# Kernel tuning notes

Hardware: AMD Instinct MI355X
Metric: run time of the kernel (lower is better)

The kernel has to match this reference:

```python
import jax, jax.numpy as jnp
import numpy as np

DIM = 1024
H = 16
DH = DIM // H
SCALE = DH ** -0.5
EPS = 1e-5


def _linear_params(key, fan_in, fan_out):
    k1, k2 = jax.random.split(key)
    bound = 1.0 / np.sqrt(fan_in)
    w = jax.random.uniform(k1, (fan_out, fan_in), jnp.float32, -bound, bound)
    b = jax.random.uniform(k2, (fan_out,), jnp.float32, -bound, bound)
    return w, b


def setup_inputs() -> dict:
    key = jax.random.key(0)
    ks = jax.random.split(key, 16)
    M, K, S_txt, S_img = 32, 128, 1024, 768
    inp = {
        'entity_text': jax.random.normal(ks[0], (M, K, DIM), jnp.float32),
        'entity_image': jax.random.normal(ks[1], (M, K, DIM), jnp.float32),
        'img_feat': jax.random.normal(ks[2], (M, S_img, DIM), jnp.float32),
        'txt_feat': jax.random.normal(ks[3], (M, S_txt, DIM), jnp.float32),
    }
    img_mask = jax.random.randint(ks[4], (M, S_img), 0, 2, jnp.int32)
    txt_mask = jax.random.randint(ks[5], (M, S_txt), 0, 2, jnp.int32)
    # guarantee at least one valid kv token per row (avoids all -inf rows)
    inp['img_mask'] = img_mask.at[:, 0].set(1)
    inp['txt_mask'] = txt_mask.at[:, 0].set(1)
    names = ['wq_t', 'wk_t', 'wv_t', 'wo_t', 'wq_i', 'wk_i', 'wv_i', 'wo_i']
    for i, n in enumerate(names):
        w, b = _linear_params(ks[6 + i], DIM, DIM)
        inp[n] = w
        inp['b' + n[1:]] = b
    inp['g_t'] = jnp.ones((DIM,), jnp.float32)
    inp['beta_t'] = jnp.zeros((DIM,), jnp.float32)
    inp['g_i'] = jnp.ones((DIM,), jnp.float32)
    inp['beta_i'] = jnp.zeros((DIM,), jnp.float32)
    return inp


def _attend(wq, bq, wk, bk, wv, bv, wo, bo, queries, kv, kv_mask):
    M, K, D = queries.shape
    S = kv.shape[1]
    Q = (queries @ wq.T + bq).reshape(M, K, H, DH)
    Kt = (kv @ wk.T + bk).reshape(M, S, H, DH)
    V = (kv @ wv.T + bv).reshape(M, S, H, DH)
    attn = jnp.einsum('mkhd,mshd->mhks', Q, Kt) * SCALE  # [M,H,K,S]
    attn = jnp.where(kv_mask[:, None, None, :] > 0, attn, -jnp.inf)
    attn = jax.nn.softmax(attn, axis=-1)
    attn = jnp.nan_to_num(attn, nan=0.0)  # dropout=eval mode (identity)
    out = jnp.einsum('mhks,mshd->mkhd', attn, V).reshape(M, K, D)
    return out @ wo.T + bo


def _layernorm(x, g, b):
    mu = jnp.mean(x, axis=-1, keepdims=True)
    var = jnp.mean(jnp.square(x - mu), axis=-1, keepdims=True)
    return (x - mu) * jax.lax.rsqrt(var + EPS) * g + b


def reference(entity_text, entity_image, img_feat, txt_feat, img_mask, txt_mask,
              wq_t, bq_t, wk_t, bk_t, wv_t, bv_t, wo_t, bo_t,
              wq_i, bq_i, wk_i, bk_i, wv_i, bv_i, wo_i, bo_i,
              g_t, beta_t, g_i, beta_i):
    out_t = _attend(wq_t, bq_t, wk_t, bk_t, wv_t, bv_t, wo_t, bo_t,
                    entity_text, txt_feat, txt_mask)
    out_i = _attend(wq_i, bq_i, wk_i, bk_i, wv_i, bv_i, wo_i, bo_i,
                    entity_image, img_feat, img_mask)
    et = _layernorm(entity_text + out_t, g_t, beta_t)
    ei = _layernorm(entity_image + out_i, g_i, beta_i)
    return (et, ei)
```

## Files before the change

### kernel.cpp

```cpp
#include <hip/hip_runtime.h>
#include <stdint.h>

typedef unsigned short u16;
typedef __attribute__((ext_vector_type(8))) short short8;
typedef __attribute__((ext_vector_type(4))) float f32x4;

#define SWZ(r) (((r) & 7) << 4)
#define SWZV(dr) ((((dr) & 7) ^ (((dr) >> 3) & 7)) << 4)
#define SCALE 0.125f

__device__ __forceinline__ u16 f2bf(float f) {
  unsigned int x = __float_as_uint(f);
  x += 0x7fffu + ((x >> 16) & 1u);
  return (u16)(x >> 16);
}

__device__ __forceinline__ unsigned int cvtpk_bf16(float lo, float hi) {
  unsigned int r;
  asm("v_cvt_pk_bf16_f32 %0, %1, %2" : "=v"(r) : "v"(lo), "v"(hi));
  return r;
}

__device__ __forceinline__ f32x4 mfma16(short8 a, short8 b, f32x4 c) {
  return __builtin_amdgcn_mfma_f32_16x16x32_bf16(a, b, c, 0, 0, 0);
}

__device__ __forceinline__ void gload_lds16(const u16* g, u16* l) {
  __builtin_amdgcn_global_load_lds(
      (const __attribute__((address_space(1))) unsigned int*)g,
      (__attribute__((address_space(3))) unsigned int*)l, 16, 0, 0);
}

__device__ __forceinline__ int xcd_swz(int bid, int nwg) {
  int cpx = nwg >> 3;
  return (bid & 7) * cpx + (bid >> 3);
}

__device__ __forceinline__ void cvt8(const float* src, u16* dst) {
  f32x4 a = __builtin_nontemporal_load((const f32x4*)src);
  f32x4 b = __builtin_nontemporal_load((const f32x4*)(src + 4));
  uint4 u;
  u.x = cvtpk_bf16(a[0], a[1]);
  u.y = cvtpk_bf16(a[2], a[3]);
  u.z = cvtpk_bf16(b[0], b[1]);
  u.w = cvtpk_bf16(b[2], b[3]);
  *(uint4*)dst = u;
}

__global__ __launch_bounds__(256) void cvt_all_kernel(
    const float* __restrict__ w0, const float* __restrict__ w1,
    const float* __restrict__ w2, const float* __restrict__ w3,
    const float* __restrict__ ent, const float* __restrict__ feat,
    u16* __restrict__ Wbf, u16* __restrict__ entbf, u16* __restrict__ featbf,
    int nE8, int nF8) {
  const int nW8 = 524288;
  int total = nW8 + nE8 + nF8;
  int i = blockIdx.x * 256 + threadIdx.x;
  int stride = gridDim.x * 256;
  for (; i < total; i += stride) {
    if (i < nW8) {
      int mi = i >> 17;
      const float* s = (mi == 0) ? w0 : (mi == 1) ? w1 : (mi == 2) ? w2 : w3;
      size_t off = (size_t)(i & 131071) * 8;
      cvt8(s + off, Wbf + (size_t)mi * 1048576 + off);
    } else if (i < nW8 + nE8) {
      size_t off = (size_t)(i - nW8) * 8;
      cvt8(ent + off, entbf + off);
    } else {
      size_t off = (size_t)(i - nW8 - nE8) * 8;
      cvt8(feat + off, featbf + off);
    }
  }
}

__global__ __launch_bounds__(256) void cvt_a_kernel(
    const float* __restrict__ src, u16* __restrict__ dst, int n8) {
  int i = blockIdx.x * 256 + threadIdx.x;
  int stride = gridDim.x * 256;
  for (; i < n8; i += stride) cvt8(src + (size_t)i * 8, dst + (size_t)i * 8);
}

__device__ __forceinline__ void gemm_core_bf16(
    const u16* __restrict__ A, const u16* __restrict__ B,
    const float* __restrict__ bias0, const float* __restrict__ bias1,
    u16* __restrict__ C, int ldc, int bx, int by, u16* As, u16* Bs) {
  const int tid = threadIdx.x;
  const int lane = tid & 63;
  const int w = tid >> 6;
  const int wr = w >> 1, wc = w & 1;
  const int l15 = lane & 15, lg = lane >> 4;
  const int brow = by * 128;
  const int bcol = bx * 128;

  f32x4 acc[4][4] = {};

  for (int k0 = 0; k0 < 1024; k0 += 64) {
#pragma unroll
    for (int p = 0; p < 4; ++p) {
      int flat = p * 256 + tid;
      int row = flat >> 3;
      int cb = (flat & 7) * 16;
      int scb = cb ^ SWZ(row);
      gload_lds16(B + (size_t)(bcol + row) * 1024 + k0 + (scb >> 1),
                  Bs + (size_t)flat * 8);
    }
#pragma unroll
    for (int p = 0; p < 4; ++p) {
      int flat = p * 256 + tid;
      int row = flat >> 3;
      int cb = (flat & 7) * 16;
      int scb = cb ^ SWZ(row);
      gload_lds16(A + (size_t)(brow + row) * 1024 + k0 + (scb >> 1),
                  As + (size_t)flat * 8);
    }
    __syncthreads();

    short8 af[4][2], bfr[4][2];
#pragma unroll
    for (int i = 0; i < 4; ++i) {
#pragma unroll
      for (int kk = 0; kk < 2; ++kk) {
        int ar = wr * 64 + i * 16 + l15;
        af[i][kk] = *(const short8*)((const char*)As + ar * 128 +
                                     ((kk * 64 + lg * 16) ^ SWZ(ar)));
        int br = wc * 64 + i * 16 + l15;
        bfr[i][kk] = *(const short8*)((const char*)Bs + br * 128 +
                                      ((kk * 64 + lg * 16) ^ SWZ(br)));
      }
    }
#pragma unroll
    for (int i = 0; i < 4; ++i)
#pragma unroll
      for (int j = 0; j < 4; ++j)
#pragma unroll
        for (int kk = 0; kk < 2; ++kk)
          acc[i][j] = mfma16(af[i][kk], bfr[j][kk], acc[i][j]);
    __syncthreads();
  }

#pragma unroll
  for (int j = 0; j < 4; ++j) {
    int col = bcol + wc * 64 + j * 16 + l15;
    const float* bp = (col < 1024) ? bias0 : bias1;
    float bv = bp[col & 1023];
#pragma unroll
    for (int i = 0; i < 4; ++i) {
      int row0 = brow + wr * 64 + i * 16 + lg * 4;
#pragma unroll
      for (int r = 0; r < 4; ++r)
        C[(size_t)(row0 + r) * ldc + col] = f2bf(acc[i][j][r] + bv);
    }
  }
}

__global__ __launch_bounds__(256, 2) void qkv_gemm_kernel(
    const u16* __restrict__ A0, const u16* __restrict__ B0,
    const float* __restrict__ bq, u16* __restrict__ C0, int gx0, int nwg0,
    const u16* __restrict__ A1, const u16* __restrict__ B1,
    const float* __restrict__ bk, const float* __restrict__ bv,
    u16* __restrict__ C1, int gx1, int nwg1) {
  __shared__ __attribute__((aligned(16))) u16 As[128 * 64];
  __shared__ __attribute__((aligned(16))) u16 Bs[128 * 64];
  int bid = blockIdx.x;
  if (bid < nwg0) {
    int lid = xcd_swz(bid, nwg0);
    gemm_core_bf16(A0, B0, bq, bq, C0, 1024, lid % gx0, lid / gx0, As, Bs);
  } else {
    int lid = xcd_swz(bid - nwg0, nwg1);
    gemm_core_bf16(A1, B1, bk, bv, C1, 2048, lid % gx1, lid / gx1, As, Bs);
  }
}

template <bool A_F32, bool OUT_F32>
__global__ __launch_bounds__(256, 2) void gemm_bias_kernel(
    const void* __restrict__ Av, const u16* __restrict__ B,
    const float* __restrict__ bias0, const float* __restrict__ bias1,
    void* __restrict__ Cv, int ldc) {
  __shared__ __attribute__((aligned(16))) u16 As[128 * 64];
  __shared__ __attribute__((aligned(16))) u16 Bs[128 * 64];
  const int tid = threadIdx.x;
  const int lane = tid & 63;
  const int w = tid >> 6;
  const int wr = w >> 1, wc = w & 1;
  const int l15 = lane & 15, lg = lane >> 4;

  const int nwg = gridDim.x * gridDim.y;
  const int lid = xcd_swz(blockIdx.y * gridDim.x + blockIdx.x, nwg);
  const int bx = lid % gridDim.x;
  const int by = lid / gridDim.x;
  const int brow = by * 128;
  const int bcol = bx * 128;

  f32x4 acc[4][4] = {};

  for (int k0 = 0; k0 < 1024; k0 += 64) {
#pragma unroll
    for (int p = 0; p < 4; ++p) {
      int flat = p * 256 + tid;
      int row = flat >> 3;
      int cb = (flat & 7) * 16;
      int scb = cb ^ SWZ(row);
      gload_lds16(B + (size_t)(bcol + row) * 1024 + k0 + (scb >> 1),
                  Bs + (size_t)flat * 8);
    }
    if constexpr (A_F32) {
      const float* Af = (const float*)Av;
#pragma unroll
      for (int p = 0; p < 4; ++p) {
        int flat = p * 256 + tid;
        int row = flat >> 3;
        int c8 = flat & 7;
        const float* src = Af + (size_t)(brow + row) * 1024 + k0 + c8 * 8;
        float4 v0 = ((const float4*)src)[0];
        float4 v1 = ((const float4*)src)[1];
        uint4 u;
        u.x = cvtpk_bf16(v0.x, v0.y);
        u.y = cvtpk_bf16(v0.z, v0.w);
        u.z = cvtpk_bf16(v1.x, v1.y);
        u.w = cvtpk_bf16(v1.z, v1.w);
        *(uint4*)((char*)As + row * 128 + ((c8 * 16) ^ SWZ(row))) = u;
      }
    } else {
      const u16* Ab = (const u16*)Av;
#pragma unroll
      for (int p = 0; p < 4; ++p) {
        int flat = p * 256 + tid;
        int row = flat >> 3;
        int cb = (flat & 7) * 16;
        int scb = cb ^ SWZ(row);
        gload_lds16(Ab + (size_t)(brow + row) * 1024 + k0 + (scb >> 1),
                    As + (size_t)flat * 8);
      }
    }
    __syncthreads();

    short8 af[4][2], bfr[4][2];
#pragma unroll
    for (int i = 0; i < 4; ++i) {
#pragma unroll
      for (int kk = 0; kk < 2; ++kk) {
        int ar = wr * 64 + i * 16 + l15;
        af[i][kk] = *(const short8*)((const char*)As + ar * 128 +
                                     ((kk * 64 + lg * 16) ^ SWZ(ar)));
        int br = wc * 64 + i * 16 + l15;
        bfr[i][kk] = *(const short8*)((const char*)Bs + br * 128 +
                                      ((kk * 64 + lg * 16) ^ SWZ(br)));
      }
    }
#pragma unroll
    for (int i = 0; i < 4; ++i)
#pragma unroll
      for (int j = 0; j < 4; ++j)
#pragma unroll
        for (int kk = 0; kk < 2; ++kk)
          acc[i][j] = mfma16(af[i][kk], bfr[j][kk], acc[i][j]);
    __syncthreads();
  }

#pragma unroll
  for (int j = 0; j < 4; ++j) {
    int col = bcol + wc * 64 + j * 16 + l15;
    const float* bp = (col < 1024) ? bias0 : bias1;
    float bv = bp[col & 1023];
#pragma unroll
    for (int i = 0; i < 4; ++i) {
      int row0 = brow + wr * 64 + i * 16 + lg * 4;
#pragma unroll
      for (int r = 0; r < 4; ++r) {
        float v = acc[i][j][r] + bv;
        if constexpr (OUT_F32)
          ((float*)Cv)[(size_t)(row0 + r) * ldc + col] = v;
        else
          ((u16*)Cv)[(size_t)(row0 + r) * ldc + col] = f2bf(v);
      }
    }
  }
}

__global__ __launch_bounds__(256, 2) void attn_mfma_kernel(
    const u16* __restrict__ Q, const u16* __restrict__ KV,
    const int* __restrict__ mask, u16* __restrict__ AO, int S, int mbase) {
  __shared__ __attribute__((aligned(16))) u16 Ks[64 * 64];
  __shared__ __attribute__((aligned(16))) u16 Vt[64 * 64];
  __shared__ __attribute__((aligned(16))) u16 Ps[4 * 32 * 64];
  __shared__ float mb[64];

  const int tid = threadIdx.x;
  const int lane = tid & 63;
  const int w = tid >> 6;
  const int lid = xcd_swz(blockIdx.x, gridDim.x);
  const int ml = lid >> 4;
  const int h = lid & 15;
  const int mg = mbase + ml;
  const int l15 = lane & 15, lg = lane >> 4;

  short8 qf[2][2];
#pragma unroll
  for (int qb = 0; qb < 2; ++qb)
#pragma unroll
    for (int kk = 0; kk < 2; ++kk)
      qf[qb][kk] = *(const short8*)(Q + (size_t)(mg * 128 + w * 32 + qb * 16 + l15) * 1024 +
                                    h * 64 + kk * 32 + lg * 8);

  float mrun[2][4], lrun[2][4];
  f32x4 oacc[2][4] = {};
#pragma unroll
  for (int qb = 0; qb < 2; ++qb)
#pragma unroll
    for (int r = 0; r < 4; ++r) {
      mrun[qb][r] = -1e30f;
      lrun[qb][r] = 0.0f;
    }

  const size_t kvbase = (size_t)ml * S * 2048 + h * 64;

  for (int st = 0; st < S; st += 64) {
    if (tid < 64)
      mb[tid] = (mask[(size_t)mg * S + st + tid] > 0) ? 0.0f : -1e30f;
#pragma unroll
    for (int p = 0; p < 2; ++p) {
      int flat = p * 256 + tid;
      int row = flat >> 3;
      int c = flat & 7;
      short8 v = *(const short8*)(KV + kvbase + (size_t)(st + row) * 2048 + c * 8);
      *(short8*)((char*)Ks + row * 128 + ((c * 16) ^ SWZ(row))) = v;
    }
    {
      int sp = (tid >> 3) * 2;
      int c = tid & 7;
      const u16* src = KV + kvbase + 1024 + (size_t)(st + sp) * 2048 + c * 8;
      short8 v0 = *(const short8*)(src);
      short8 v1 = *(const short8*)(src + 2048);
#pragma unroll
      for (int j = 0; j < 8; ++j) {
        int dr = c * 8 + j;
        unsigned int val = (unsigned int)(u16)v0[j] | ((unsigned int)(u16)v1[j] << 16);
        *(unsigned int*)((char*)Vt + dr * 128 + ((sp * 2) ^ SWZV(dr))) = val;
      }
    }
    __syncthreads();

    short8 kf[4][2];
#pragma unroll
    for (int sb = 0; sb < 4; ++sb)
#pragma unroll
      for (int kk = 0; kk < 2; ++kk) {
        int row = sb * 16 + l15;
        kf[sb][kk] = *(const short8*)((const char*)Ks + row * 128 +
                                      ((kk * 64 + lg * 16) ^ SWZ(row)));
      }
    f32x4 sc[2][4] = {};
#pragma unroll
    for (int qb = 0; qb < 2; ++qb)
#pragma unroll
      for (int sb = 0; sb < 4; ++sb)
#pragma unroll
        for (int kk = 0; kk < 2; ++kk)
          sc[qb][sb] = mfma16(qf[qb][kk], kf[sb][kk], sc[qb][sb]);

    float mbv[4];
#pragma unroll
    for (int sb = 0; sb < 4; ++sb) mbv[sb] = mb[sb * 16 + l15];

#pragma unroll
    for (int qb = 0; qb < 2; ++qb) {
#pragma unroll
      for (int r = 0; r < 4; ++r) {
        float s0 = sc[qb][0][r] * SCALE + mbv[0];
        float s1 = sc[qb][1][r] * SCALE + mbv[1];
        float s2 = sc[qb][2][r] * SCALE + mbv[2];
        float s3 = sc[qb][3][r] * SCALE + mbv[3];
        float t = fmaxf(fmaxf(s0, s1), fmaxf(s2, s3));
        for (int d = 1; d < 16; d <<= 1) t = fmaxf(t, __shfl_xor(t, d));
        float mnew = fmaxf(mrun[qb][r], t);
        float resc = __expf(mrun[qb][r] - mnew);
        float p0 = __expf(s0 - mnew);
        float p1 = __expf(s1 - mnew);
        float p2 = __expf(s2 - mnew);
        float p3 = __expf(s3 - mnew);
        float rs = p0 + p1 + p2 + p3;
        for (int d = 1; d < 16; d <<= 1) rs += __shfl_xor(rs, d);
        lrun[qb][r] = lrun[qb][r] * resc + rs;
        mrun[qb][r] = mnew;
#pragma unroll
        for (int db = 0; db < 4; ++db) oacc[qb][db][r] *= resc;
        int row = qb * 16 + lg * 4 + r;
        char* pbase = (char*)Ps + (w * 32 + row) * 128;
        int colb = 2 * l15;
        *(u16*)(pbase + ((0 * 32 + colb) ^ SWZ(row))) = f2bf(p0);
        *(u16*)(pbase + ((1 * 32 + colb) ^ SWZ(row))) = f2bf(p1);
        *(u16*)(pbase + ((2 * 32 + colb) ^ SWZ(row))) = f2bf(p2);
        *(u16*)(pbase + ((3 * 32 + colb) ^ SWZ(row))) = f2bf(p3);
      }
    }
    asm volatile("" ::: "memory");

    short8 pf[2][2], vf[4][2];
#pragma unroll
    for (int qb = 0; qb < 2; ++qb)
#pragma unroll
      for (int kk = 0; kk < 2; ++kk) {
        int row = qb * 16 + l15;
        pf[qb][kk] = *(const short8*)((const char*)Ps + (w * 32 + row) * 128 +
                                      ((kk * 64 + lg * 16) ^ SWZ(row)));
      }
#pragma unroll
    for (int db = 0; db < 4; ++db)
#pragma unroll
      for (int kk = 0; kk < 2; ++kk) {
        int row = db * 16 + l15;
        vf[db][kk] = *(const short8*)((const char*)Vt + row * 128 +
                                      ((kk * 64 + lg * 16) ^ SWZV(row)));
      }
#pragma unroll
    for (int qb = 0; qb < 2; ++qb)
#pragma unroll
      for (int db = 0; db < 4; ++db)
#pragma unroll
        for (int kk = 0; kk < 2; ++kk)
          oacc[qb][db] = mfma16(pf[qb][kk], vf[db][kk], oacc[qb][db]);
    __syncthreads();
  }

#pragma unroll
  for (int qb = 0; qb < 2; ++qb)
#pragma unroll
    for (int db = 0; db < 4; ++db)
#pragma unroll
      for (int r = 0; r < 4; ++r) {
        int grow = mg * 128 + w * 32 + qb * 16 + lg * 4 + r;
        int gcol = h * 64 + db * 16 + l15;
        float v = oacc[qb][db][r] / lrun[qb][r];
        AO[(size_t)grow * 1024 + gcol] = f2bf(v);
      }
}

__global__ __launch_bounds__(256) void ln_kernel(
    const float* __restrict__ X, const float* __restrict__ O,
    const float* __restrict__ g, const float* __restrict__ b,
    float* __restrict__ out) {
  int row = blockIdx.x;
  int tid = threadIdx.x;
  const float* xr = X + (size_t)row * 1024;
  const float* orr = O + (size_t)row * 1024;
  float4 xv = *(const float4*)(xr + tid * 4);
  float4 ov = *(const float4*)(orr + tid * 4);
  float v0 = xv.x + ov.x, v1 = xv.y + ov.y, v2 = xv.z + ov.z, v3 = xv.w + ov.w;
  float s = v0 + v1 + v2 + v3;
  float s2 = v0 * v0 + v1 * v1 + v2 * v2 + v3 * v3;
  for (int d = 1; d < 64; d <<= 1) {
    s += __shfl_xor(s, d);
    s2 += __shfl_xor(s2, d);
  }
  __shared__ float ps[4], ps2[4];
  int w = tid >> 6;
  if ((tid & 63) == 0) {
    ps[w] = s;
    ps2[w] = s2;
  }
  __syncthreads();
  s = ps[0] + ps[1] + ps[2] + ps[3];
  s2 = ps2[0] + ps2[1] + ps2[2] + ps2[3];
  float mu = s * (1.0f / 1024.0f);
  float var = s2 * (1.0f / 1024.0f) - mu * mu;
  float rstd = rsqrtf(var + 1e-5f);
  float4 gv = *(const float4*)(g + tid * 4);
  float4 bv = *(const float4*)(b + tid * 4);
  float4 ou;
  ou.x = (v0 - mu) * rstd * gv.x + bv.x;
  ou.y = (v1 - mu) * rstd * gv.y + bv.y;
  ou.z = (v2 - mu) * rstd * gv.z + bv.z;
  ou.w = (v3 - mu) * rstd * gv.w + bv.w;
  *(float4*)(out + (size_t)row * 1024 + tid * 4) = ou;
}

extern "C" void kernel_launch(void* const* d_in, const int* in_sizes, int n_in,
                              void* d_out, int out_size, void* d_ws, size_t ws_size,
                              hipStream_t stream) {
  const float* ent_t = (const float*)d_in[0];
  const float* ent_i = (const float*)d_in[1];
  const float* img_feat = (const float*)d_in[2];
  const float* txt_feat = (const float*)d_in[3];
  const int* img_mask = (const int*)d_in[4];
  const int* txt_mask = (const int*)d_in[5];
  const float* W[8];
  const float* Bv[8];
  for (int i = 0; i < 8; ++i) {
    W[i] = (const float*)d_in[6 + 2 * i];
    Bv[i] = (const float*)d_in[7 + 2 * i];
  }
  const float* g_t = (const float*)d_in[22];
  const float* beta_t = (const float*)d_in[23];
  const float* g_i = (const float*)d_in[24];
  const float* beta_i = (const float*)d_in[25];
  float* out = (float*)d_out;

  int nc = 0;
  size_t Xt = 0;
  for (int t = 1; t <= 4; t <<= 1) {
    size_t x = 134217728ull / t;
    if ((32ull << 20) + x + x / 2 <= ws_size) { nc = t; Xt = x; break; }
  }

  char* ws = (char*)d_ws;
  u16* Wbf = (u16*)ws;
  u16* Qbf = (u16*)(ws + (8ull << 20));
  u16* AObf = (u16*)(ws + (16ull << 20));

  if (nc > 0) {
    u16* entbf = (u16*)(ws + (24ull << 20));
    u16* KVc = (u16*)(ws + (32ull << 20));
    u16* featbf = (u16*)(ws + (32ull << 20) + Xt);
    float* Of32 = (float*)(ws + (32ull << 20));
    const int mpc = 32 / nc;

    for (int mod = 0; mod < 2; ++mod) {
      const float* ent = mod ? ent_i : ent_t;
      const float* feat = mod ? img_feat : txt_feat;
      const int* msk = mod ? img_mask : txt_mask;
      int S = mod ? 768 : 1024;
      int crows = mpc * S;

      const u16* wq = Wbf;
      const u16* wkv = Wbf + 1ull * 1048576;
      const u16* wo = Wbf + 3ull * 1048576;

      cvt_all_kernel<<<2048, 256, 0, stream>>>(
          W[mod * 4 + 0], W[mod * 4 + 1], W[mod * 4 + 2], W[mod * 4 + 3],
          ent, feat, Wbf, entbf, featbf, 4096 * 128, crows * 128);

      for (int c = 0; c < nc; ++c) {
        if (c > 0) {
          const float* featc = feat + (size_t)c * mpc * S * 1024;
          cvt_a_kernel<<<2048, 256, 0, stream>>>(featc, featbf, crows * 128);
        }
        int nwg0 = (c == 0) ? 256 : 0;
        int nwg1 = 16 * (crows / 128);
        qkv_gemm_kernel<<<nwg0 + nwg1, 256, 0, stream>>>(
            entbf, wq, Bv[mod * 4 + 0], Qbf, 8, nwg0,
            featbf, wkv, Bv[mod * 4 + 1], Bv[mod * 4 + 2], KVc, 16, nwg1);
        attn_mfma_kernel<<<mpc * 16, 256, 0, stream>>>(Qbf, KVc, msk, AObf, S, c * mpc);
      }

      gemm_bias_kernel<false, true><<<dim3(8, 32), 256, 0, stream>>>(
          AObf, wo, Bv[mod * 4 + 3], Bv[mod * 4 + 3], Of32, 1024);
      ln_kernel<<<4096, 256, 0, stream>>>(ent, Of32,
                                          mod ? g_i : g_t, mod ? beta_i : beta_t,
                                          out + (size_t)mod * 4194304);
    }
  } else {
    int ncf = 4;
    if (ws_size >= (152ull << 20)) ncf = 1;
    else if (ws_size >= (88ull << 20)) ncf = 2;
    u16* KVc = (u16*)(ws + (24ull << 20));
    float* Of32 = (float*)(ws + (24ull << 20));
    const int mpc = 32 / ncf;

    for (int mod = 0; mod < 2; ++mod) {
      const float* ent = mod ? ent_i : ent_t;
      const float* feat = mod ? img_feat : txt_feat;
      const int* msk = mod ? img_mask : txt_mask;
      int S = mod ? 768 : 1024;

      cvt_all_kernel<<<2048, 256, 0, stream>>>(
          W[mod * 4 + 0], W[mod * 4 + 1], W[mod * 4 + 2], W[mod * 4 + 3],
          ent, ent, Wbf, Qbf, Qbf, 0, 0);

      const u16* wq = Wbf;
      const u16* wkv = Wbf + 1ull * 1048576;
      const u16* wo = Wbf + 3ull * 1048576;

      gemm_bias_kernel<true, false><<<dim3(8, 32), 256, 0, stream>>>(
          ent, wq, Bv[mod * 4 + 0], Bv[mod * 4 + 0], Qbf, 1024);

      int crows = mpc * S;
      for (int c = 0; c < ncf; ++c) {
        const float* featc = feat + (size_t)c * mpc * S * 1024;
        gemm_bias_kernel<true, false><<<dim3(16, crows / 128), 256, 0, stream>>>(
            featc, wkv, Bv[mod * 4 + 1], Bv[mod * 4 + 2], KVc, 2048);
        attn_mfma_kernel<<<mpc * 16, 256, 0, stream>>>(Qbf, KVc, msk, AObf, S, c * mpc);
      }

      gemm_bias_kernel<false, true><<<dim3(8, 32), 256, 0, stream>>>(
          AObf, wo, Bv[mod * 4 + 3], Bv[mod * 4 + 3], Of32, 1024);
      ln_kernel<<<4096, 256, 0, stream>>>(ent, Of32,
                                          mod ? g_i : g_t, mod ? beta_i : beta_t,
                                          out + (size_t)mod * 4194304);
    }
  }
}
```

Measured before the change: 511.8 us.

## Add large-workspace path batching both modalities' output projection and layernorm

When the workspace is large enough, a new path runs each modality's convert, QKV GEMM and attention without chunking. It keeps separate attention-output buffers per modality so that both output projections run in one combined launch and both layernorms in another. The aim is fewer kernel launches and a better-filled grid for the small output-projection GEMMs. In exchange it needs at least 240 MB of workspace, and the old chunked path remains as the fallback.

```diff
diff --git a/kernel.cpp b/kernel.cpp
--- a/kernel.cpp
+++ b/kernel.cpp
@@ -80,10 +80,11 @@
   for (; i < n8; i += stride) cvt8(src + (size_t)i * 8, dst + (size_t)i * 8);
 }
 
-__device__ __forceinline__ void gemm_core_bf16(
+template <bool OUT_F32>
+__device__ __forceinline__ void gemm_core(
     const u16* __restrict__ A, const u16* __restrict__ B,
     const float* __restrict__ bias0, const float* __restrict__ bias1,
-    u16* __restrict__ C, int ldc, int bx, int by, u16* As, u16* Bs) {
+    void* __restrict__ Cv, int ldc, int bx, int by, u16* As, u16* Bs) {
   const int tid = threadIdx.x;
   const int lane = tid & 63;
   const int w = tid >> 6;
@@ -99,8 +100,7 @@
     for (int p = 0; p < 4; ++p) {
       int flat = p * 256 + tid;
       int row = flat >> 3;
-      int cb = (flat & 7) * 16;
-      int scb = cb ^ SWZ(row);
+      int scb = ((flat & 7) * 16) ^ SWZ(row);
       gload_lds16(B + (size_t)(bcol + row) * 1024 + k0 + (scb >> 1),
                   Bs + (size_t)flat * 8);
     }
@@ -108,8 +108,7 @@
     for (int p = 0; p < 4; ++p) {
       int flat = p * 256 + tid;
       int row = flat >> 3;
-      int cb = (flat & 7) * 16;
-      int scb = cb ^ SWZ(row);
+      int scb = ((flat & 7) * 16) ^ SWZ(row);
       gload_lds16(A + (size_t)(brow + row) * 1024 + k0 + (scb >> 1),
                   As + (size_t)flat * 8);
     }
@@ -147,8 +146,13 @@
     for (int i = 0; i < 4; ++i) {
       int row0 = brow + wr * 64 + i * 16 + lg * 4;
 #pragma unroll
-      for (int r = 0; r < 4; ++r)
-        C[(size_t)(row0 + r) * ldc + col] = f2bf(acc[i][j][r] + bv);
+      for (int r = 0; r < 4; ++r) {
+        float v = acc[i][j][r] + bv;
+        if constexpr (OUT_F32)
+          ((float*)Cv)[(size_t)(row0 + r) * ldc + col] = v;
+        else
+          ((u16*)Cv)[(size_t)(row0 + r) * ldc + col] = f2bf(v);
+      }
     }
   }
 }
@@ -164,10 +168,27 @@
   int bid = blockIdx.x;
   if (bid < nwg0) {
     int lid = xcd_swz(bid, nwg0);
-    gemm_core_bf16(A0, B0, bq, bq, C0, 1024, lid % gx0, lid / gx0, As, Bs);
+    gemm_core<false>(A0, B0, bq, bq, C0, 1024, lid % gx0, lid / gx0, As, Bs);
   } else {
     int lid = xcd_swz(bid - nwg0, nwg1);
-    gemm_core_bf16(A1, B1, bk, bv, C1, 2048, lid % gx1, lid / gx1, As, Bs);
+    gemm_core<false>(A1, B1, bk, bv, C1, 2048, lid % gx1, lid / gx1, As, Bs);
+  }
+}
+
+__global__ __launch_bounds__(256, 2) void wo2_kernel(
+    const u16* __restrict__ A0, const u16* __restrict__ B0,
+    const float* __restrict__ b0, float* __restrict__ C0, int n0,
+    const u16* __restrict__ A1, const u16* __restrict__ B1,
+    const float* __restrict__ b1, float* __restrict__ C1) {
+  __shared__ __attribute__((aligned(16))) u16 As[128 * 64];
+  __shared__ __attribute__((aligned(16))) u16 Bs[128 * 64];
+  int bid = blockIdx.x;
+  if (bid < n0) {
+    int lid = xcd_swz(bid, n0);
+    gemm_core<true>(A0, B0, b0, b0, C0, 1024, lid % 8, lid / 8, As, Bs);
+  } else {
+    int lid = xcd_swz(bid - n0, gridDim.x - n0);
+    gemm_core<true>(A1, B1, b1, b1, C1, 1024, lid % 8, lid / 8, As, Bs);
   }
 }
 
@@ -179,31 +200,31 @@
   __shared__ __attribute__((aligned(16))) u16 As[128 * 64];
   __shared__ __attribute__((aligned(16))) u16 Bs[128 * 64];
   const int tid = threadIdx.x;
-  const int lane = tid & 63;
-  const int w = tid >> 6;
-  const int wr = w >> 1, wc = w & 1;
-  const int l15 = lane & 15, lg = lane >> 4;
-
   const int nwg = gridDim.x * gridDim.y;
   const int lid = xcd_swz(blockIdx.y * gridDim.x + blockIdx.x, nwg);
   const int bx = lid % gridDim.x;
   const int by = lid / gridDim.x;
-  const int brow = by * 128;
-  const int bcol = bx * 128;
-
-  f32x4 acc[4][4] = {};
-
-  for (int k0 = 0; k0 < 1024; k0 += 64) {
-#pragma unroll
-    for (int p = 0; p < 4; ++p) {
-      int flat = p * 256 + tid;
-      int row = flat >> 3;
-      int cb = (flat & 7) * 16;
-      int scb = cb ^ SWZ(row);
-      gload_lds16(B + (size_t)(bcol + row) * 1024 + k0 + (scb >> 1),
-                  Bs + (size_t)flat * 8);
-    }
-    if constexpr (A_F32) {
+
+  if constexpr (!A_F32) {
+    gemm_core<OUT_F32>((const u16*)Av, B, bias0, bias1, Cv, ldc, bx, by, As, Bs);
+    return;
+  } else {
+    const int lane = tid & 63;
+    const int w = tid >> 6;
+    const int wr = w >> 1, wc = w & 1;
+    const int l15 = lane & 15, lg = lane >> 4;
+    const int brow = by * 128;
+    const int bcol = bx * 128;
+    f32x4 acc[4][4] = {};
+    for (int k0 = 0; k0 < 1024; k0 += 64) {
+#pragma unroll
+      for (int p = 0; p < 4; ++p) {
+        int flat = p * 256 + tid;
+        int row = flat >> 3;
+        int scb = ((flat & 7) * 16) ^ SWZ(row);
+        gload_lds16(B + (size_t)(bcol + row) * 1024 + k0 + (scb >> 1),
+                    Bs + (size_t)flat * 8);
+      }
       const float* Af = (const float*)Av;
 #pragma unroll
       for (int p = 0; p < 4; ++p) {
@@ -220,58 +241,45 @@
         u.w = cvtpk_bf16(v1.z, v1.w);
         *(uint4*)((char*)As + row * 128 + ((c8 * 16) ^ SWZ(row))) = u;
       }
-    } else {
-      const u16* Ab = (const u16*)Av;
-#pragma unroll
-      for (int p = 0; p < 4; ++p) {
-        int flat = p * 256 + tid;
-        int row = flat >> 3;
-        int cb = (flat & 7) * 16;
-        int scb = cb ^ SWZ(row);
-        gload_lds16(Ab + (size_t)(brow + row) * 1024 + k0 + (scb >> 1),
-                    As + (size_t)flat * 8);
-      }
-    }
-    __syncthreads();
-
-    short8 af[4][2], bfr[4][2];
-#pragma unroll
-    for (int i = 0; i < 4; ++i) {
-#pragma unroll
-      for (int kk = 0; kk < 2; ++kk) {
-        int ar = wr * 64 + i * 16 + l15;
-        af[i][kk] = *(const short8*)((const char*)As + ar * 128 +
-                                     ((kk * 64 + lg * 16) ^ SWZ(ar)));
-        int br = wc * 64 + i * 16 + l15;
-        bfr[i][kk] = *(const short8*)((const char*)Bs + br * 128 +
-                                      ((kk * 64 + lg * 16) ^ SWZ(br)));
-      }
-    }
-#pragma unroll
-    for (int i = 0; i < 4; ++i)
-#pragma unroll
-      for (int j = 0; j < 4; ++j)
-#pragma unroll
-        for (int kk = 0; kk < 2; ++kk)
-          acc[i][j] = mfma16(af[i][kk], bfr[j][kk], acc[i][j]);
-    __syncthreads();
-  }
-
-#pragma unroll
-  for (int j = 0; j < 4; ++j) {
-    int col = bcol + wc * 64 + j * 16 + l15;
-    const float* bp = (col < 1024) ? bias0 : bias1;
-    float bv = bp[col & 1023];
-#pragma unroll
-    for (int i = 0; i < 4; ++i) {
-      int row0 = brow + wr * 64 + i * 16 + lg * 4;
-#pragma unroll
-      for (int r = 0; r < 4; ++r) {
-        float v = acc[i][j][r] + bv;
-        if constexpr (OUT_F32)
-          ((float*)Cv)[(size_t)(row0 + r) * ldc + col] = v;
-        else
-          ((u16*)Cv)[(size_t)(row0 + r) * ldc + col] = f2bf(v);
+      __syncthreads();
+      short8 af[4][2], bfr[4][2];
+#pragma unroll
+      for (int i = 0; i < 4; ++i) {
+#pragma unroll
+        for (int kk = 0; kk < 2; ++kk) {
+          int ar = wr * 64 + i * 16 + l15;
+          af[i][kk] = *(const short8*)((const char*)As + ar * 128 +
+                                       ((kk * 64 + lg * 16) ^ SWZ(ar)));
+          int br = wc * 64 + i * 16 + l15;
+          bfr[i][kk] = *(const short8*)((const char*)Bs + br * 128 +
+                                        ((kk * 64 + lg * 16) ^ SWZ(br)));
+        }
+      }
+#pragma unroll
+      for (int i = 0; i < 4; ++i)
+#pragma unroll
+        for (int j = 0; j < 4; ++j)
+#pragma unroll
+          for (int kk = 0; kk < 2; ++kk)
+            acc[i][j] = mfma16(af[i][kk], bfr[j][kk], acc[i][j]);
+      __syncthreads();
+    }
+#pragma unroll
+    for (int j = 0; j < 4; ++j) {
+      int col = bcol + wc * 64 + j * 16 + l15;
+      const float* bp = (col < 1024) ? bias0 : bias1;
+      float bv = bp[col & 1023];
+#pragma unroll
+      for (int i = 0; i < 4; ++i) {
+        int row0 = brow + wr * 64 + i * 16 + lg * 4;
+#pragma unroll
+        for (int r = 0; r < 4; ++r) {
+          float v = acc[i][j][r] + bv;
+          if constexpr (OUT_F32)
+            ((float*)Cv)[(size_t)(row0 + r) * ldc + col] = v;
+          else
+            ((u16*)Cv)[(size_t)(row0 + r) * ldc + col] = f2bf(v);
+        }
       }
     }
   }
@@ -435,11 +443,10 @@
       }
 }
 
-__global__ __launch_bounds__(256) void ln_kernel(
+__device__ __forceinline__ void ln_core(
     const float* __restrict__ X, const float* __restrict__ O,
     const float* __restrict__ g, const float* __restrict__ b,
-    float* __restrict__ out) {
-  int row = blockIdx.x;
+    float* __restrict__ out, int row) {
   int tid = threadIdx.x;
   const float* xr = X + (size_t)row * 1024;
   const float* orr = O + (size_t)row * 1024;
@@ -474,6 +481,26 @@
   *(float4*)(out + (size_t)row * 1024 + tid * 4) = ou;
 }
 
+__global__ __launch_bounds__(256) void ln_kernel(
+    const float* __restrict__ X, const float* __restrict__ O,
+    const float* __restrict__ g, const float* __restrict__ b,
+    float* __restrict__ out) {
+  ln_core(X, O, g, b, out, blockIdx.x);
+}
+
+__global__ __launch_bounds__(256) void ln2_kernel(
+    const float* __restrict__ X0, const float* __restrict__ O0,
+    const float* __restrict__ g0, const float* __restrict__ b0,
+    const float* __restrict__ X1, const float* __restrict__ O1,
+    const float* __restrict__ g1, const float* __restrict__ b1,
+    float* __restrict__ out) {
+  int row = blockIdx.x;
+  if (row < 4096)
+    ln_core(X0, O0, g0, b0, out, row);
+  else
+    ln_core(X1, O1, g1, b1, out + 4194304, row - 4096);
+}
+
 extern "C" void kernel_launch(void* const* d_in, const int* in_sizes, int n_in,
                               void* d_out, int out_size, void* d_ws, size_t ws_size,
                               hipStream_t stream) {
@@ -494,6 +521,52 @@
   const float* g_i = (const float*)d_in[24];
   const float* beta_i = (const float*)d_in[25];
   float* out = (float*)d_out;
+  char* ws = (char*)d_ws;
+
+  if (ws_size >= (240ull << 20)) {
+    u16* Wbf = (u16*)ws;
+    u16* Qbf = (u16*)(ws + (16ull << 20));
+    u16* AObf_t = (u16*)(ws + (24ull << 20));
+    u16* AObf_i = (u16*)(ws + (32ull << 20));
+    u16* entbf = (u16*)(ws + (40ull << 20));
+    u16* KVc = (u16*)(ws + (48ull << 20));
+    u16* featbf = (u16*)(ws + (176ull << 20));
+    float* Of32_t = (float*)(ws + (48ull << 20));
+    float* Of32_i = (float*)(ws + (48ull << 20) + (16ull << 20));
+
+    for (int mod = 0; mod < 2; ++mod) {
+      const float* ent = mod ? ent_i : ent_t;
+      const float* feat = mod ? img_feat : txt_feat;
+      const int* msk = mod ? img_mask : txt_mask;
+      u16* AObf = mod ? AObf_i : AObf_t;
+      int S = mod ? 768 : 1024;
+      int crows = 32 * S;
+
+      const u16* wq = Wbf + (size_t)mod * 4 * 1048576;
+      const u16* wkv = Wbf + ((size_t)mod * 4 + 1) * 1048576;
+
+      cvt_all_kernel<<<2048, 256, 0, stream>>>(
+          W[mod * 4 + 0], W[mod * 4 + 1], W[mod * 4 + 2], W[mod * 4 + 3],
+          ent, feat, Wbf + (size_t)mod * 4 * 1048576, entbf, featbf,
+          4096 * 128, crows * 128);
+
+      qkv_gemm_kernel<<<256 + 16 * (crows / 128), 256, 0, stream>>>(
+          entbf, wq, Bv[mod * 4 + 0], Qbf, 8, 256,
+          featbf, wkv, Bv[mod * 4 + 1], Bv[mod * 4 + 2], KVc, 16,
+          16 * (crows / 128));
+
+      attn_mfma_kernel<<<512, 256, 0, stream>>>(Qbf, KVc, msk, AObf, S, 0);
+    }
+
+    wo2_kernel<<<512, 256, 0, stream>>>(
+        AObf_t, Wbf + 3ull * 1048576, Bv[3], Of32_t, 256,
+        AObf_i, Wbf + 7ull * 1048576, Bv[7], Of32_i);
+
+    ln2_kernel<<<8192, 256, 0, stream>>>(
+        ent_t, Of32_t, g_t, beta_t,
+        ent_i, Of32_i, g_i, beta_i, out);
+    return;
+  }
 
   int nc = 0;
   size_t Xt = 0;
@@ -502,7 +575,6 @@
     if ((32ull << 20) + x + x / 2 <= ws_size) { nc = t; Xt = x; break; }
   }
 
-  char* ws = (char*)d_ws;
   u16* Wbf = (u16*)ws;
   u16* Qbf = (u16*)(ws + (8ull << 20));
   u16* AObf = (u16*)(ws + (16ull << 20));
```

Result: faster. 493.1 us, median of 2 (-3.7%).
